# Kernel tuning notes

Measured on AMD Instinct MI355X. Metric: run time of the kernel, lower is better.

## Reference

```python
import jax, jax.numpy as jnp
import numpy as np

B_, L_, D_MODEL = 4, 1024, 768
D_STATE, D_CONV, EXPAND = 16, 4, 2
D_INNER = EXPAND * D_MODEL
DT_RANK = int(np.ceil(D_MODEL / 16))
EPS = 1e-5


def setup_inputs() -> dict:
    key = jax.random.key(0)
    ks = jax.random.split(key, 8)
    s = 0.02
    hidden_states = jax.random.normal(ks[0], (B_, L_, D_MODEL), jnp.float32)
    norm_w = jnp.ones((D_MODEL,), jnp.float32)
    in_proj_w = jax.random.normal(ks[1], (2 * D_INNER, D_MODEL), jnp.float32) * s
    conv_w = jax.random.normal(ks[2], (D_INNER, D_CONV), jnp.float32) * 0.1  # depthwise kernel
    conv_b = jnp.zeros((D_INNER,), jnp.float32)
    x_proj_w = jax.random.normal(ks[3], (DT_RANK + 2 * D_STATE, D_INNER), jnp.float32) * s
    dt_std = DT_RANK ** -0.5
    dt_proj_w = jax.random.uniform(ks[4], (D_INNER, DT_RANK), jnp.float32, -dt_std, dt_std)
    # A_log init: log(1..d_state) repeated over d_inner, as in source
    A_log = jnp.log(jnp.tile(jnp.arange(1, D_STATE + 1, dtype=jnp.float32), (D_INNER, 1)))
    D_param = jnp.ones((D_INNER,), jnp.float32)
    out_proj_w = jax.random.normal(ks[5], (D_MODEL, D_INNER), jnp.float32) * s
    return dict(hidden_states=hidden_states, norm_w=norm_w, in_proj_w=in_proj_w,
                conv_w=conv_w, conv_b=conv_b, x_proj_w=x_proj_w, dt_proj_w=dt_proj_w,
                A_log=A_log, D_param=D_param, out_proj_w=out_proj_w)


def _causal_dwconv(x, w, b):
    # x: (b, l, d); w: (d, k). torch Conv1d(groups=d, padding=k-1)[..., :L] == causal conv.
    k = w.shape[1]
    L = x.shape[1]
    xp = jnp.pad(x, ((0, 0), (k - 1, 0), (0, 0)))
    out = xp[:, 0:L, :] * w[:, 0]
    for i in range(1, k):
        out = out + xp[:, i:i + L, :] * w[:, i]
    return out + b


def reference(hidden_states, norm_w, in_proj_w, conv_w, conv_b, x_proj_w,
              dt_proj_w, A_log, D_param, out_proj_w):
    residual = hidden_states
    # RMSNorm
    h = hidden_states * jax.lax.rsqrt(jnp.mean(hidden_states ** 2, -1, keepdims=True) + EPS) * norm_w
    # in_proj -> split x, z
    xz = h @ in_proj_w.T                      # (b, l, 2*d_inner)
    x, z = jnp.split(xz, 2, axis=-1)          # each (b, l, d_inner)
    # causal depthwise conv + SiLU
    x = jax.nn.silu(_causal_dwconv(x, conv_w, conv_b))
    # x_proj -> dt, B, C
    x_dbl = x @ x_proj_w.T                    # (b, l, dt_rank + 2*d_state)
    dt, Bm, Cm = jnp.split(x_dbl, [DT_RANK, DT_RANK + D_STATE], axis=-1)
    dt = dt @ dt_proj_w.T                     # (b, l, d_inner); NOTE: no bias, matches source
    A = -jnp.exp(A_log)                       # (d_inner, d_state)
    # selective scan; softplus applied only in deltaA (matches source), raw dt in deltaB_u
    dA = jnp.exp(jax.nn.softplus(dt)[..., None] * A)        # (b, l, d, n)
    dBu = (dt * x)[..., None] * Bm[:, :, None, :]            # (b, l, d, n)

    def step(hst, inp):
        dA_t, dBu_t, C_t = inp
        hst = dA_t * hst + dBu_t               # (b, d, n)
        y_t = jnp.einsum('bdn,bn->bd', hst, C_t)
        return hst, y_t

    h0 = jnp.zeros((x.shape[0], D_INNER, D_STATE), x.dtype)
    _, ys = jax.lax.scan(step, h0, (dA.transpose(1, 0, 2, 3), dBu.transpose(1, 0, 2, 3), Cm.transpose(1, 0, 2)))
    y = ys.transpose(1, 0, 2) + x * D_param    # (b, l, d_inner)
    y = y * jax.nn.silu(z)
    out = y @ out_proj_w.T                     # (b, l, d_model)
    return residual + out
```

## Files before the change

kernel.cpp:

```cpp
#include <hip/hip_runtime.h>
#include <hip/hip_bf16.h>
#include <math.h>


#define BB 4
#define LL 1024
#define DMODEL 768
#define DSTATE 16
#define DINNER 1536
#define DTRANK 48
#define NROWS (BB*LL)
#define EPSF 1e-5f
#define NCHUNK 32
#define CLEN 32
#define DGRPS (DINNER/256)
#define XP_SPLITK 4
#define XPK (DINNER/XP_SPLITK)

typedef __attribute__((ext_vector_type(8))) short bf16x8;
typedef __attribute__((ext_vector_type(8))) ushort ushort8;
typedef __attribute__((ext_vector_type(4))) float f32x4;

__device__ __forceinline__ float softplus_f(float x) {
    return (x > 20.f) ? x : __logf(1.f + __expf(x));
}
__device__ __forceinline__ float silu_f(float x) {
    return x / (1.f + __expf(-x));
}
__device__ __forceinline__ ushort f2bf(float x) {
    union { float f; uint32_t u; } v; v.f = x;
    uint32_t r = v.u + 0x7FFF + ((v.u >> 16) & 1);
    return (ushort)(r >> 16);
}
__device__ __forceinline__ float bf2f(ushort u) {
    union { uint32_t u; float f; } v; v.u = ((uint32_t)u) << 16;
    return v.f;
}

__global__ __launch_bounds__(256) void f32_to_bf16_x8(const float* __restrict__ in,
                                                      ushort* __restrict__ out, int n8) {
    int i = blockIdx.x * 256 + threadIdx.x;
    if (i >= n8) return;
    const float4* ip = reinterpret_cast<const float4*>(in) + (size_t)i * 2;
    float4 v0 = ip[0], v1 = ip[1];
    uint4 o;
    o.x = (uint32_t)f2bf(v0.x) | ((uint32_t)f2bf(v0.y) << 16);
    o.y = (uint32_t)f2bf(v0.z) | ((uint32_t)f2bf(v0.w) << 16);
    o.z = (uint32_t)f2bf(v1.x) | ((uint32_t)f2bf(v1.y) << 16);
    o.w = (uint32_t)f2bf(v1.z) | ((uint32_t)f2bf(v1.w) << 16);
    reinterpret_cast<uint4*>(out)[i] = o;
}

__global__ __launch_bounds__(256) void rmsnorm_kernel(const float* __restrict__ x,
                                                      const float* __restrict__ w,
                                                      ushort* __restrict__ out) {
    int wave = threadIdx.x >> 6;
    int lane = threadIdx.x & 63;
    int row  = blockIdx.x * 4 + wave;
    const float4* xr = reinterpret_cast<const float4*>(x + (size_t)row * DMODEL);
    const float4* wr = reinterpret_cast<const float4*>(w);
    float4 v[3];
    float ss = 0.f;
#pragma unroll
    for (int i = 0; i < 3; i++) {
        v[i] = xr[lane + i * 64];
        ss += v[i].x*v[i].x + v[i].y*v[i].y + v[i].z*v[i].z + v[i].w*v[i].w;
    }
#pragma unroll
    for (int m = 1; m < 64; m <<= 1) ss += __shfl_xor(ss, m);
    float scale = rsqrtf(ss * (1.0f / DMODEL) + EPSF);
    ushort4* orow = reinterpret_cast<ushort4*>(out + (size_t)row * DMODEL);
#pragma unroll
    for (int i = 0; i < 3; i++) {
        float4 wv = wr[lane + i * 64];
        ushort4 o;
        o.x = f2bf(v[i].x * scale * wv.x);
        o.y = f2bf(v[i].y * scale * wv.y);
        o.z = f2bf(v[i].z * scale * wv.z);
        o.w = f2bf(v[i].w * scale * wv.w);
        orow[lane + i * 64] = o;
    }
}

__global__ __launch_bounds__(256) void gemm_bf16_bt(
        const ushort* __restrict__ A, int lda,
        const ushort* __restrict__ W, int ldw,
        const float* __restrict__ Res,
        float* __restrict__ C, ushort* __restrict__ Cbf,
        int ldc, int K) {
    __shared__ ushort As[128 * 32];
    __shared__ ushort Bs[128 * 32];
    int t = threadIdx.x;
    int m0 = blockIdx.y * 128, n0 = blockIdx.x * 128;
    int srow = t >> 2;
    int scol = (t & 3) * 8;
    int lane = t & 63;
    int wid  = t >> 6;
    int wr = wid >> 1, wc = wid & 1;
    int fr = lane & 15;
    int fq = lane >> 4;

    const ushort* Ap = A + (size_t)(m0 + srow) * lda + scol;
    const ushort* Wp = W + (size_t)(n0 + srow) * ldw + scol;
    int sdst = srow * 32 + scol;

    int aoff[4], boff[4];
#pragma unroll
    for (int m = 0; m < 4; m++) aoff[m] = (wr * 64 + m * 16 + fr) * 32 + fq * 8;
#pragma unroll
    for (int n = 0; n < 4; n++) boff[n] = (wc * 64 + n * 16 + fr) * 32 + fq * 8;

    f32x4 acc[4][4];
#pragma unroll
    for (int m = 0; m < 4; m++)
#pragma unroll
        for (int n = 0; n < 4; n++)
#pragma unroll
            for (int r = 0; r < 4; r++) acc[m][n][r] = 0.f;

    for (int k0 = 0; k0 < K; k0 += 32) {
        uint4 a0 = *reinterpret_cast<const uint4*>(Ap + k0);
        uint4 a1 = *reinterpret_cast<const uint4*>(Ap + (size_t)64 * lda + k0);
        uint4 b0 = *reinterpret_cast<const uint4*>(Wp + k0);
        uint4 b1 = *reinterpret_cast<const uint4*>(Wp + (size_t)64 * ldw + k0);
        __syncthreads();
        *reinterpret_cast<uint4*>(&As[sdst])            = a0;
        *reinterpret_cast<uint4*>(&As[sdst + 64 * 32])  = a1;
        *reinterpret_cast<uint4*>(&Bs[sdst])            = b0;
        *reinterpret_cast<uint4*>(&Bs[sdst + 64 * 32])  = b1;
        __syncthreads();
        bf16x8 af[4], bfr[4];
#pragma unroll
        for (int m = 0; m < 4; m++) af[m] = *reinterpret_cast<const bf16x8*>(&As[aoff[m]]);
#pragma unroll
        for (int n = 0; n < 4; n++) bfr[n] = *reinterpret_cast<const bf16x8*>(&Bs[boff[n]]);
#pragma unroll
        for (int m = 0; m < 4; m++)
#pragma unroll
            for (int n = 0; n < 4; n++)
                acc[m][n] = __builtin_amdgcn_mfma_f32_16x16x32_bf16(af[m], bfr[n], acc[m][n], 0, 0, 0);
    }

#pragma unroll
    for (int m = 0; m < 4; m++) {
#pragma unroll
        for (int n = 0; n < 4; n++) {
            int col = n0 + wc * 64 + n * 16 + fr;
#pragma unroll
            for (int r = 0; r < 4; r++) {
                int row = m0 + wr * 64 + m * 16 + fq * 4 + r;
                float v = acc[m][n][r];
                if (Cbf) {
                    Cbf[(size_t)row * ldc + col] = f2bf(v);
                } else {
                    if (Res) v += Res[(size_t)row * ldc + col];
                    C[(size_t)row * ldc + col] = v;
                }
            }
        }
    }
}

__global__ __launch_bounds__(256) void xproj_gemm(const ushort* __restrict__ Xc,
                                                  const ushort* __restrict__ Wx,
                                                  float* __restrict__ part) {
    int ks = blockIdx.x;
    int m0 = blockIdx.y * 64;
    int wid = threadIdx.x >> 6;
    int lane = threadIdx.x & 63;
    int fr = lane & 15, fq = lane >> 4;
    const ushort* Ap = Xc + (size_t)(m0 + wid * 16 + fr) * DINNER + fq * 8 + ks * XPK;
    const ushort* Wp = Wx + (size_t)fr * DINNER + fq * 8 + ks * XPK;
    f32x4 acc[5];
#pragma unroll
    for (int ct = 0; ct < 5; ct++)
#pragma unroll
        for (int r = 0; r < 4; r++) acc[ct][r] = 0.f;
    for (int k = 0; k < XPK; k += 32) {
        bf16x8 a = *reinterpret_cast<const bf16x8*>(Ap + k);
#pragma unroll
        for (int ct = 0; ct < 5; ct++) {
            bf16x8 b = *reinterpret_cast<const bf16x8*>(Wp + (size_t)ct * 16 * DINNER + k);
            acc[ct] = __builtin_amdgcn_mfma_f32_16x16x32_bf16(a, b, acc[ct], 0, 0, 0);
        }
    }
    float* pbase = part + (size_t)ks * (NROWS * 80);
#pragma unroll
    for (int ct = 0; ct < 5; ct++)
#pragma unroll
        for (int r = 0; r < 4; r++)
            pbase[(size_t)(m0 + wid * 16 + fq * 4 + r) * 80 + ct * 16 + fr] = acc[ct][r];
}

__global__ __launch_bounds__(256) void xproj_reduce(const float* __restrict__ part,
                                                    float* __restrict__ xdbl) {
    int i = blockIdx.x * 256 + threadIdx.x;
    const float4* p4 = reinterpret_cast<const float4*>(part);
    float4 s = p4[i];
#pragma unroll
    for (int k = 1; k < XP_SPLITK; k++) {
        float4 v = p4[i + (size_t)k * (NROWS * 80 / 4)];
        s.x += v.x; s.y += v.y; s.z += v.z; s.w += v.w;
    }
    reinterpret_cast<float4*>(xdbl)[i] = s;
}

__global__ __launch_bounds__(256) void gemm_bt(const float* __restrict__ A, int lda,
                                               const float* __restrict__ W, int ldw,
                                               const float* __restrict__ Res,
                                               float* __restrict__ C, int ldc,
                                               int M, int N, int K) {
    __shared__ float As[16][68];
    __shared__ float Ws[16][68];
    int tid = threadIdx.x;
    int tx = tid & 15, ty = tid >> 4;
    int m0 = blockIdx.y * 64, n0 = blockIdx.x * 64;
    int lrow = tid >> 2;
    int lk   = (tid & 3) * 4;
    int arow = m0 + lrow;
    int wrow = n0 + lrow;
    bool wvalid = (wrow < N);
    float acc[4][4] = {};

    for (int k0 = 0; k0 < K; k0 += 16) {
        float4 av = *reinterpret_cast<const float4*>(A + (size_t)arow * lda + k0 + lk);
        float4 wv = wvalid ? *reinterpret_cast<const float4*>(W + (size_t)wrow * ldw + k0 + lk)
                           : make_float4(0.f, 0.f, 0.f, 0.f);
        __syncthreads();
        As[lk+0][lrow] = av.x; As[lk+1][lrow] = av.y; As[lk+2][lrow] = av.z; As[lk+3][lrow] = av.w;
        Ws[lk+0][lrow] = wv.x; Ws[lk+1][lrow] = wv.y; Ws[lk+2][lrow] = wv.z; Ws[lk+3][lrow] = wv.w;
        __syncthreads();
#pragma unroll
        for (int kk = 0; kk < 16; kk++) {
            float4 a = *reinterpret_cast<const float4*>(&As[kk][ty * 4]);
            float4 w = *reinterpret_cast<const float4*>(&Ws[kk][tx * 4]);
            acc[0][0] += a.x * w.x; acc[0][1] += a.x * w.y; acc[0][2] += a.x * w.z; acc[0][3] += a.x * w.w;
            acc[1][0] += a.y * w.x; acc[1][1] += a.y * w.y; acc[1][2] += a.y * w.z; acc[1][3] += a.y * w.w;
            acc[2][0] += a.z * w.x; acc[2][1] += a.z * w.y; acc[2][2] += a.z * w.z; acc[2][3] += a.z * w.w;
            acc[3][0] += a.w * w.x; acc[3][1] += a.w * w.y; acc[3][2] += a.w * w.z; acc[3][3] += a.w * w.w;
        }
    }

#pragma unroll
    for (int i = 0; i < 4; i++) {
        int row = m0 + ty * 4 + i;
        int col = n0 + tx * 4;
        if (col < N) {
            float4 o = make_float4(acc[i][0], acc[i][1], acc[i][2], acc[i][3]);
            if (Res) {
                float4 r = *reinterpret_cast<const float4*>(Res + (size_t)row * ldc + col);
                o.x += r.x; o.y += r.y; o.z += r.z; o.w += r.w;
            }
            *reinterpret_cast<float4*>(C + (size_t)row * ldc + col) = o;
        }
    }
}

__global__ __launch_bounds__(256) void conv_silu_kernel(const ushort* __restrict__ xz,
                                                        const float* __restrict__ cw,
                                                        const float* __restrict__ cb,
                                                        ushort* __restrict__ out) {
    int i = blockIdx.x * 256 + threadIdx.x;
    int d8 = i % (DINNER / 8);
    int ml = i / (DINNER / 8);
    int l  = ml % LL;
    int d  = d8 * 8;
    ushort8 xv[4];
#pragma unroll
    for (int tap = 0; tap < 4; tap++) {
        int li = l - 3 + tap;
        if (li >= 0) xv[tap] = *reinterpret_cast<const ushort8*>(xz + (size_t)(ml - 3 + tap) * 3072 + d);
        else {
            ushort8 z = {0,0,0,0,0,0,0,0};
            xv[tap] = z;
        }
    }
    const float4* cw4 = reinterpret_cast<const float4*>(cw);
    ushort8 o;
#pragma unroll
    for (int j = 0; j < 8; j++) {
        float4 w = cw4[d + j];
        float acc = cb[d + j] + bf2f(xv[0][j]) * w.x + bf2f(xv[1][j]) * w.y
                  + bf2f(xv[2][j]) * w.z + bf2f(xv[3][j]) * w.w;
        o[j] = f2bf(silu_f(acc));
    }
    *reinterpret_cast<ushort8*>(out + (size_t)ml * DINNER + d) = o;
}

__global__ __launch_bounds__(256) void scan_pass1(
        const float* __restrict__ dt, const ushort* __restrict__ xc,
        const float* __restrict__ xdbl, const float* __restrict__ A_log,
        float* __restrict__ hend, float* __restrict__ ssp) {
    __shared__ float Bs[CLEN][DSTATE];
    int tid = threadIdx.x;
    int dgrp = blockIdx.x % DGRPS;
    int chunk = (blockIdx.x / DGRPS) % NCHUNK;
    int b = blockIdx.x / (DGRPS * NCHUNK);
    int d = dgrp * 256 + tid;
    int rbase = b * LL + chunk * CLEN;
    for (int idx = tid; idx < CLEN * DSTATE; idx += 256) {
        int t = idx >> 4, j = idx & 15;
        Bs[t][j] = xdbl[(size_t)(rbase + t) * 80 + DTRANK + j];
    }
    float a[16];
    const float4* ar = reinterpret_cast<const float4*>(A_log + (size_t)d * 16);
#pragma unroll
    for (int i = 0; i < 4; i++) {
        float4 v = ar[i];
        a[4*i+0] = -__expf(v.x); a[4*i+1] = -__expf(v.y);
        a[4*i+2] = -__expf(v.z); a[4*i+3] = -__expf(v.w);
    }
    __syncthreads();
    float h[16];
#pragma unroll
    for (int n = 0; n < 16; n++) h[n] = 0.f;
    float sum_sp = 0.f;
    for (int t = 0; t < CLEN; t++) {
        int rm = rbase + t;
        float dtv = dt[(size_t)rm * DINNER + d];
        float xv  = bf2f(xc[(size_t)rm * DINNER + d]);
        float sp  = softplus_f(dtv);
        sum_sp += sp;
        float du = dtv * xv;
#pragma unroll
        for (int n = 0; n < 16; n++)
            h[n] = __expf(sp * a[n]) * h[n] + du * Bs[t][n];
    }
    size_t o = (size_t)(b * NCHUNK + chunk) * DINNER + d;
    float4* ho = reinterpret_cast<float4*>(hend + o * 16);
#pragma unroll
    for (int i = 0; i < 4; i++)
        ho[i] = make_float4(h[4*i], h[4*i+1], h[4*i+2], h[4*i+3]);
    ssp[o] = sum_sp;
}

__global__ __launch_bounds__(256) void scan_pass2(
        const float* __restrict__ hend, const float* __restrict__ ssp,
        const float* __restrict__ A_log, float* __restrict__ hini) {
    int g = blockIdx.x * 256 + threadIdx.x;
    int n = g & 15;
    int d = (g >> 4) % DINNER;
    int b = g / (16 * DINNER);
    float a = -__expf(A_log[(size_t)d * 16 + n]);
    float h = 0.f;
    for (int c = 0; c < NCHUNK; c++) {
        size_t o = (size_t)(b * NCHUNK + c) * DINNER + d;
        hini[o * 16 + n] = h;
        h = __expf(a * ssp[o]) * h + hend[o * 16 + n];
    }
}

__global__ __launch_bounds__(256) void scan_pass3(
        const float* __restrict__ dt, const ushort* __restrict__ xc,
        const float* __restrict__ xdbl, const float* __restrict__ A_log,
        const float* __restrict__ Dp, const ushort* __restrict__ xz,
        const float* __restrict__ hini, ushort* __restrict__ y) {
    __shared__ float BCs[CLEN][2*DSTATE];
    int tid = threadIdx.x;
    int dgrp = blockIdx.x % DGRPS;
    int chunk = (blockIdx.x / DGRPS) % NCHUNK;
    int b = blockIdx.x / (DGRPS * NCHUNK);
    int d = dgrp * 256 + tid;
    int rbase = b * LL + chunk * CLEN;
    for (int idx = tid; idx < CLEN * 2 * DSTATE; idx += 256) {
        int t = idx >> 5, j = idx & 31;
        BCs[t][j] = xdbl[(size_t)(rbase + t) * 80 + DTRANK + j];
    }
    float a[16];
    const float4* ar = reinterpret_cast<const float4*>(A_log + (size_t)d * 16);
#pragma unroll
    for (int i = 0; i < 4; i++) {
        float4 v = ar[i];
        a[4*i+0] = -__expf(v.x); a[4*i+1] = -__expf(v.y);
        a[4*i+2] = -__expf(v.z); a[4*i+3] = -__expf(v.w);
    }
    float dD = Dp[d];
    float h[16];
    size_t o = (size_t)(b * NCHUNK + chunk) * DINNER + d;
    const float4* hi = reinterpret_cast<const float4*>(hini + o * 16);
#pragma unroll
    for (int i = 0; i < 4; i++) {
        float4 v = hi[i];
        h[4*i] = v.x; h[4*i+1] = v.y; h[4*i+2] = v.z; h[4*i+3] = v.w;
    }
    __syncthreads();
    for (int t = 0; t < CLEN; t++) {
        int rm = rbase + t;
        float dtv = dt[(size_t)rm * DINNER + d];
        float xv  = bf2f(xc[(size_t)rm * DINNER + d]);
        float zv  = bf2f(xz[(size_t)rm * 3072 + DINNER + d]);
        float sp  = softplus_f(dtv);
        float du  = dtv * xv;
        float acc = 0.f;
#pragma unroll
        for (int n = 0; n < 16; n++) {
            h[n] = __expf(sp * a[n]) * h[n] + du * BCs[t][n];
            acc += h[n] * BCs[t][DSTATE + n];
        }
        y[(size_t)rm * DINNER + d] = f2bf((acc + xv * dD) * silu_f(zv));
    }
}

extern "C" void kernel_launch(void* const* d_in, const int* in_sizes, int n_in,
                              void* d_out, int out_size, void* d_ws, size_t ws_size,
                              hipStream_t stream) {
    const float* hs        = (const float*)d_in[0];
    const float* norm_w    = (const float*)d_in[1];
    const float* in_proj_w = (const float*)d_in[2];
    const float* conv_w    = (const float*)d_in[3];
    const float* conv_b    = (const float*)d_in[4];
    const float* x_proj_w  = (const float*)d_in[5];
    const float* dt_proj_w = (const float*)d_in[6];
    const float* A_log     = (const float*)d_in[7];
    const float* D_param   = (const float*)d_in[8];
    const float* out_proj_w= (const float*)d_in[9];
    float* out = (float*)d_out;

    float* ws = (float*)d_ws;
    ushort* h_bf = (ushort*)ws;
    float*  hend = ws;
    ushort* xz_bf    = (ushort*)(ws + 3145728);
    ushort* xconv_bf = (ushort*)(ws + 9437184);
    float* xdbl  = ws + 12582912;
    float* xpart = ws + 12910592;
    float* dtb   = ws + 14221312;
    ushort* y_bf = (ushort*)(ws + 20512768);
    float* hini  = ws + 23658496;
    float* ssp   = ws + 26804224;
    ushort* w_in_bf  = (ushort*)(ws + 27000832);
    ushort* w_out_bf = (ushort*)(ws + 28180480);
    ushort* w_x_bf   = (ushort*)(ws + 28770304);

    f32_to_bf16_x8<<<(294912 + 255)/256, 256, 0, stream>>>(in_proj_w, w_in_bf, 294912);
    f32_to_bf16_x8<<<(147456 + 255)/256, 256, 0, stream>>>(out_proj_w, w_out_bf, 147456);
    f32_to_bf16_x8<<<(15360 + 255)/256, 256, 0, stream>>>(x_proj_w, w_x_bf, 15360);

    rmsnorm_kernel<<<NROWS / 4, 256, 0, stream>>>(hs, norm_w, h_bf);
    gemm_bf16_bt<<<dim3(3072/128, NROWS/128), 256, 0, stream>>>(
        h_bf, DMODEL, w_in_bf, DMODEL, nullptr, nullptr, xz_bf, 2 * DINNER, DMODEL);
    conv_silu_kernel<<<(NROWS * DINNER / 8) / 256, 256, 0, stream>>>(
        xz_bf, conv_w, conv_b, xconv_bf);
    xproj_gemm<<<dim3(XP_SPLITK, NROWS/64), 256, 0, stream>>>(xconv_bf, w_x_bf, xpart);
    xproj_reduce<<<(NROWS * 80 / 4) / 256, 256, 0, stream>>>(xpart, xdbl);
    gemm_bt<<<dim3(DINNER / 64, NROWS / 64), 256, 0, stream>>>(
        xdbl, 80, dt_proj_w, DTRANK, nullptr, dtb, DINNER, NROWS, DINNER, DTRANK);
    scan_pass1<<<BB * NCHUNK * DGRPS, 256, 0, stream>>>(dtb, xconv_bf, xdbl, A_log, hend, ssp);
    scan_pass2<<<(BB * DINNER * DSTATE) / 256, 256, 0, stream>>>(hend, ssp, A_log, hini);
    scan_pass3<<<BB * NCHUNK * DGRPS, 256, 0, stream>>>(dtb, xconv_bf, xdbl, A_log, D_param,
                                                        xz_bf, hini, y_bf);
    gemm_bf16_bt<<<dim3(DMODEL/128, NROWS/128), 256, 0, stream>>>(
        y_bf, DINNER, w_out_bf, DINNER, hs, out, nullptr, DMODEL, DINNER);
}
```

Measured before the change: 303.4 us.

## Split-K out_proj GEMM with residual reduce and direct global-to-LDS loads

The out_proj GEMM now splits K four ways, so its grid grows from 192 to 768 blocks and fills more compute units. Partial sums go to a workspace buffer, and a separate reduce kernel adds them together with the residual. Both bf16 GEMMs also switch to global_load_lds, which loads tiles straight into shared memory instead of staging them through registers. The cost is extra global traffic for the partials and one more kernel launch, and the direct LDS load relies on the lane-to-address mapping matching the expected tile layout.

```diff
diff --git a/kernel.cpp b/kernel.cpp
--- a/kernel.cpp
+++ b/kernel.cpp
@@ -16,6 +16,8 @@
 #define DGRPS (DINNER/256)
 #define XP_SPLITK 4
 #define XPK (DINNER/XP_SPLITK)
+#define OP_SPLITK 4
+#define OPK (DINNER/OP_SPLITK)
 
 typedef __attribute__((ext_vector_type(8))) short bf16x8;
 typedef __attribute__((ext_vector_type(8))) ushort ushort8;
@@ -35,6 +37,11 @@
 __device__ __forceinline__ float bf2f(ushort u) {
     union { uint32_t u; float f; } v; v.u = ((uint32_t)u) << 16;
     return v.f;
+}
+__device__ __forceinline__ void gload16(const ushort* g, ushort* l) {
+    __builtin_amdgcn_global_load_lds(
+        (const __attribute__((address_space(1))) unsigned int*)g,
+        (__attribute__((address_space(3))) unsigned int*)l, 16, 0, 0);
 }
 
 __global__ __launch_bounds__(256) void f32_to_bf16_x8(const float* __restrict__ in,
@@ -85,9 +92,7 @@
 __global__ __launch_bounds__(256) void gemm_bf16_bt(
         const ushort* __restrict__ A, int lda,
         const ushort* __restrict__ W, int ldw,
-        const float* __restrict__ Res,
-        float* __restrict__ C, ushort* __restrict__ Cbf,
-        int ldc, int K) {
+        ushort* __restrict__ Cbf, int ldc, int K) {
     __shared__ ushort As[128 * 32];
     __shared__ ushort Bs[128 * 32];
     int t = threadIdx.x;
@@ -102,7 +107,6 @@
 
     const ushort* Ap = A + (size_t)(m0 + srow) * lda + scol;
     const ushort* Wp = W + (size_t)(n0 + srow) * ldw + scol;
-    int sdst = srow * 32 + scol;
 
     int aoff[4], boff[4];
 #pragma unroll
@@ -119,15 +123,11 @@
             for (int r = 0; r < 4; r++) acc[m][n][r] = 0.f;
 
     for (int k0 = 0; k0 < K; k0 += 32) {
-        uint4 a0 = *reinterpret_cast<const uint4*>(Ap + k0);
-        uint4 a1 = *reinterpret_cast<const uint4*>(Ap + (size_t)64 * lda + k0);
-        uint4 b0 = *reinterpret_cast<const uint4*>(Wp + k0);
-        uint4 b1 = *reinterpret_cast<const uint4*>(Wp + (size_t)64 * ldw + k0);
         __syncthreads();
-        *reinterpret_cast<uint4*>(&As[sdst])            = a0;
-        *reinterpret_cast<uint4*>(&As[sdst + 64 * 32])  = a1;
-        *reinterpret_cast<uint4*>(&Bs[sdst])            = b0;
-        *reinterpret_cast<uint4*>(&Bs[sdst + 64 * 32])  = b1;
+        gload16(Ap + k0,                    &As[wid * 512]);
+        gload16(Ap + (size_t)64 * lda + k0, &As[2048 + wid * 512]);
+        gload16(Wp + k0,                    &Bs[wid * 512]);
+        gload16(Wp + (size_t)64 * ldw + k0, &Bs[2048 + wid * 512]);
         __syncthreads();
         bf16x8 af[4], bfr[4];
 #pragma unroll
@@ -149,16 +149,92 @@
 #pragma unroll
             for (int r = 0; r < 4; r++) {
                 int row = m0 + wr * 64 + m * 16 + fq * 4 + r;
-                float v = acc[m][n][r];
-                if (Cbf) {
-                    Cbf[(size_t)row * ldc + col] = f2bf(v);
-                } else {
-                    if (Res) v += Res[(size_t)row * ldc + col];
-                    C[(size_t)row * ldc + col] = v;
-                }
+                Cbf[(size_t)row * ldc + col] = f2bf(acc[m][n][r]);
             }
         }
     }
+}
+
+__global__ __launch_bounds__(256) void gemm_bf16_splitk(
+        const ushort* __restrict__ A, int lda,
+        const ushort* __restrict__ W, int ldw,
+        float* __restrict__ part, int N, int Kc) {
+    __shared__ ushort As[128 * 32];
+    __shared__ ushort Bs[128 * 32];
+    int t = threadIdx.x;
+    int m0 = blockIdx.y * 128, n0 = blockIdx.x * 128;
+    int kbase = blockIdx.z * Kc;
+    int srow = t >> 2;
+    int scol = (t & 3) * 8;
+    int lane = t & 63;
+    int wid  = t >> 6;
+    int wr = wid >> 1, wc = wid & 1;
+    int fr = lane & 15;
+    int fq = lane >> 4;
+
+    const ushort* Ap = A + (size_t)(m0 + srow) * lda + kbase + scol;
+    const ushort* Wp = W + (size_t)(n0 + srow) * ldw + kbase + scol;
+
+    int aoff[4], boff[4];
+#pragma unroll
+    for (int m = 0; m < 4; m++) aoff[m] = (wr * 64 + m * 16 + fr) * 32 + fq * 8;
+#pragma unroll
+    for (int n = 0; n < 4; n++) boff[n] = (wc * 64 + n * 16 + fr) * 32 + fq * 8;
+
+    f32x4 acc[4][4];
+#pragma unroll
+    for (int m = 0; m < 4; m++)
+#pragma unroll
+        for (int n = 0; n < 4; n++)
+#pragma unroll
+            for (int r = 0; r < 4; r++) acc[m][n][r] = 0.f;
+
+    for (int k0 = 0; k0 < Kc; k0 += 32) {
+        __syncthreads();
+        gload16(Ap + k0,                    &As[wid * 512]);
+        gload16(Ap + (size_t)64 * lda + k0, &As[2048 + wid * 512]);
+        gload16(Wp + k0,                    &Bs[wid * 512]);
+        gload16(Wp + (size_t)64 * ldw + k0, &Bs[2048 + wid * 512]);
+        __syncthreads();
+        bf16x8 af[4], bfr[4];
+#pragma unroll
+        for (int m = 0; m < 4; m++) af[m] = *reinterpret_cast<const bf16x8*>(&As[aoff[m]]);
+#pragma unroll
+        for (int n = 0; n < 4; n++) bfr[n] = *reinterpret_cast<const bf16x8*>(&Bs[boff[n]]);
+#pragma unroll
+        for (int m = 0; m < 4; m++)
+#pragma unroll
+            for (int n = 0; n < 4; n++)
+                acc[m][n] = __builtin_amdgcn_mfma_f32_16x16x32_bf16(af[m], bfr[n], acc[m][n], 0, 0, 0);
+    }
+
+    float* pb = part + (size_t)blockIdx.z * NROWS * N;
+#pragma unroll
+    for (int m = 0; m < 4; m++) {
+#pragma unroll
+        for (int n = 0; n < 4; n++) {
+            int col = n0 + wc * 64 + n * 16 + fr;
+#pragma unroll
+            for (int r = 0; r < 4; r++) {
+                int row = m0 + wr * 64 + m * 16 + fq * 4 + r;
+                pb[(size_t)row * N + col] = acc[m][n][r];
+            }
+        }
+    }
+}
+
+__global__ __launch_bounds__(256) void reduce4_res(const float* __restrict__ part,
+                                                   const float* __restrict__ res,
+                                                   float* __restrict__ out) {
+    int i = blockIdx.x * 256 + threadIdx.x;
+    const float4* p4 = reinterpret_cast<const float4*>(part);
+    float4 s = reinterpret_cast<const float4*>(res)[i];
+#pragma unroll
+    for (int z = 0; z < OP_SPLITK; z++) {
+        float4 v = p4[i + (size_t)z * (NROWS * DMODEL / 4)];
+        s.x += v.x; s.y += v.y; s.z += v.z; s.w += v.w;
+    }
+    reinterpret_cast<float4*>(out)[i] = s;
 }
 
 __global__ __launch_bounds__(256) void xproj_gemm(const ushort* __restrict__ Xc,
@@ -207,7 +283,6 @@
 
 __global__ __launch_bounds__(256) void gemm_bt(const float* __restrict__ A, int lda,
                                                const float* __restrict__ W, int ldw,
-                                               const float* __restrict__ Res,
                                                float* __restrict__ C, int ldc,
                                                int M, int N, int K) {
     __shared__ float As[16][68];
@@ -247,10 +322,6 @@
         int col = n0 + tx * 4;
         if (col < N) {
             float4 o = make_float4(acc[i][0], acc[i][1], acc[i][2], acc[i][3]);
-            if (Res) {
-                float4 r = *reinterpret_cast<const float4*>(Res + (size_t)row * ldc + col);
-                o.x += r.x; o.y += r.y; o.z += r.z; o.w += r.w;
-            }
             *reinterpret_cast<float4*>(C + (size_t)row * ldc + col) = o;
         }
     }
@@ -430,6 +501,7 @@
     ushort* w_in_bf  = (ushort*)(ws + 27000832);
     ushort* w_out_bf = (ushort*)(ws + 28180480);
     ushort* w_x_bf   = (ushort*)(ws + 28770304);
+    float* opart = ws + 3145728;
 
     f32_to_bf16_x8<<<(294912 + 255)/256, 256, 0, stream>>>(in_proj_w, w_in_bf, 294912);
     f32_to_bf16_x8<<<(147456 + 255)/256, 256, 0, stream>>>(out_proj_w, w_out_bf, 147456);
@@ -437,17 +509,18 @@
 
     rmsnorm_kernel<<<NROWS / 4, 256, 0, stream>>>(hs, norm_w, h_bf);
     gemm_bf16_bt<<<dim3(3072/128, NROWS/128), 256, 0, stream>>>(
-        h_bf, DMODEL, w_in_bf, DMODEL, nullptr, nullptr, xz_bf, 2 * DINNER, DMODEL);
+        h_bf, DMODEL, w_in_bf, DMODEL, xz_bf, 2 * DINNER, DMODEL);
     conv_silu_kernel<<<(NROWS * DINNER / 8) / 256, 256, 0, stream>>>(
         xz_bf, conv_w, conv_b, xconv_bf);
     xproj_gemm<<<dim3(XP_SPLITK, NROWS/64), 256, 0, stream>>>(xconv_bf, w_x_bf, xpart);
     xproj_reduce<<<(NROWS * 80 / 4) / 256, 256, 0, stream>>>(xpart, xdbl);
     gemm_bt<<<dim3(DINNER / 64, NROWS / 64), 256, 0, stream>>>(
-        xdbl, 80, dt_proj_w, DTRANK, nullptr, dtb, DINNER, NROWS, DINNER, DTRANK);
+        xdbl, 80, dt_proj_w, DTRANK, dtb, DINNER, NROWS, DINNER, DTRANK);
     scan_pass1<<<BB * NCHUNK * DGRPS, 256, 0, stream>>>(dtb, xconv_bf, xdbl, A_log, hend, ssp);
     scan_pass2<<<(BB * DINNER * DSTATE) / 256, 256, 0, stream>>>(hend, ssp, A_log, hini);
     scan_pass3<<<BB * NCHUNK * DGRPS, 256, 0, stream>>>(dtb, xconv_bf, xdbl, A_log, D_param,
                                                         xz_bf, hini, y_bf);
-    gemm_bf16_bt<<<dim3(DMODEL/128, NROWS/128), 256, 0, stream>>>(
-        y_bf, DINNER, w_out_bf, DINNER, hs, out, nullptr, DMODEL, DINNER);
-}
+    gemm_bf16_splitk<<<dim3(DMODEL/128, NROWS/128, OP_SPLITK), 256, 0, stream>>>(
+        y_bf, DINNER, w_out_bf, DINNER, opart, DMODEL, OPK);
+    reduce4_res<<<(NROWS * DMODEL / 4) / 256, 256, 0, stream>>>(opart, hs, out);
+}
```

Result: faster. 278.4 us (-8.2%).
